# Kernel optimization log

Measured on AMD Instinct MI355X. Metric: run time of the kernel, lower is better.

## Reference

```python
import jax, jax.numpy as jnp
import numpy as np

N = 100000   # nodes
E = 100000   # hyperedges
M = 1600000  # incidences
IN_C = 128
HID = 128
OUT_C = 64
L = 2
EPS = 1e-5


def _layer_norm(x, g, b):
    m = jnp.mean(x, axis=-1, keepdims=True)
    v = jnp.mean((x - m) ** 2, axis=-1, keepdims=True)
    return (x - m) * jax.lax.rsqrt(v + EPS) * g + b


def setup_inputs() -> dict:
    key = jax.random.key(0)
    ks = jax.random.split(key, 16)
    s_in = 1.0 / np.sqrt(IN_C)
    s_h = 1.0 / np.sqrt(HID)
    return {
        "x": jax.random.normal(ks[0], (N, IN_C), jnp.float32),
        "x_e": jax.random.normal(ks[1], (E, IN_C), jnp.float32),
        "edge_index": jax.random.randint(ks[2], (2, M), 0, N, jnp.int32),
        "in_norm_g": jnp.ones((IN_C,), jnp.float32),
        "in_norm_b": jnp.zeros((IN_C,), jnp.float32),
        "in_proj_W": jax.random.normal(ks[3], (IN_C, HID), jnp.float32) * s_in,
        "in_proj_b": jnp.zeros((HID,), jnp.float32),
        "norm_g": jnp.ones((L, HID), jnp.float32),
        "norm_b": jnp.zeros((L, HID), jnp.float32),
        "conv_W": jax.random.normal(ks[4], (L, HID, HID), jnp.float32) * s_h,
        "conv_b": jnp.zeros((L, HID), jnp.float32),
        "lin_W": jax.random.normal(ks[5], (HID, OUT_C), jnp.float32) * s_h,
        "lin_b": jnp.zeros((OUT_C,), jnp.float32),
    }


def reference(x, x_e, edge_index, in_norm_g, in_norm_b, in_proj_W, in_proj_b,
              norm_g, norm_b, conv_W, conv_b, lin_W, lin_b):
    src, dst = edge_index[0], edge_index[1]  # node ids, hyperedge ids
    h = _layer_norm(x, in_norm_g, in_norm_b)
    h = jax.nn.leaky_relu(h @ in_proj_W + in_proj_b)  # dropout = identity (eval)

    # HypergraphConv degree normalizers (hyperedge_weight = 1)
    ones = jnp.ones((M,), h.dtype)
    degD = jax.ops.segment_sum(ones, src, num_segments=N)
    D = jnp.where(degD > 0, 1.0 / degD, 0.0)          # [N]
    degB = jax.ops.segment_sum(ones, dst, num_segments=E)
    B = jnp.where(degB > 0, 1.0 / degB, 0.0)          # [E]

    for i in range(L):
        hn = _layer_norm(h, norm_g[i], norm_b[i])
        xw = hn @ conv_W[i]                            # [N, HID]
        # node -> hyperedge: sum_j B[e] * xw[j]
        he = jax.ops.segment_sum(B[dst][:, None] * xw[src], dst, num_segments=E)
        # hyperedge -> node: sum_e D[n] * he[e]
        h2 = jax.ops.segment_sum(D[src][:, None] * he[dst], src, num_segments=N)
        h = jax.nn.leaky_relu(h2 + conv_b[i])

    # MinAggregation: segment-min of gathered node features per hyperedge
    agg = jax.ops.segment_min(h[src], dst, num_segments=E)  # [E, HID]
    return agg @ lin_W + lin_b                              # [E, OUT_C]
```

## Files before the change

kernel.cpp:

```cpp
#include <hip/hip_runtime.h>

#define NN 100000
#define NE 100000
#define MI 1600000
#define HID 128
#define OUTC 64
#define LSLOPE 0.01f
#define EPSV 1e-5f
#define ADJ_STRIDE 48
#define BUILD_PASSES 10
#define BUILD_WIN ((NN + BUILD_PASSES - 1) / BUILD_PASSES)

typedef __attribute__((ext_vector_type(4))) unsigned short us4;
typedef __attribute__((ext_vector_type(8))) short short8;
typedef __attribute__((ext_vector_type(16))) float f32x16;

__device__ __forceinline__ float bf2f(unsigned short h) {
    return __uint_as_float(((unsigned)h) << 16);
}
__device__ __forceinline__ unsigned short f2bf(float f) {
    unsigned u = __float_as_uint(f);
    return (unsigned short)((u + 0x7FFFu + ((u >> 16) & 1u)) >> 16);
}

__global__ void build_win_kernel(const int* __restrict__ ei,
                                 int* __restrict__ cntE, int* __restrict__ cntN,
                                 int* __restrict__ adjE, int* __restrict__ adjN,
                                 int lo, int hi) {
    int m = blockIdx.x * blockDim.x + threadIdx.x;
    if (m >= MI) return;
    int s = ei[m], d = ei[MI + m];
    if (d >= lo && d < hi) {
        int p = atomicAdd(&cntE[d], 1);
        if (p < ADJ_STRIDE) adjE[d * ADJ_STRIDE + p] = s;
    }
    if (s >= lo && s < hi) {
        int p = atomicAdd(&cntN[s], 1);
        if (p < ADJ_STRIDE) adjN[s * ADJ_STRIDE + p] = d;
    }
}

__global__ void recip_kernel(const int* __restrict__ deg, float* __restrict__ out, int n) {
    int i = blockIdx.x * blockDim.x + threadIdx.x;
    if (i < n) { int d = deg[i]; out[i] = d > 0 ? 1.0f / (float)d : 0.0f; }
}

__global__ void tconv_kernel(const float* __restrict__ src, unsigned short* __restrict__ hi,
                             unsigned short* __restrict__ lo, int K, int N) {
    int idx = blockIdx.x * blockDim.x + threadIdx.x;
    if (idx >= K * N) return;
    int n = idx / K, k = idx - n * K;
    float v = src[k * N + n];
    unsigned short h = f2bf(v);
    hi[idx] = h;
    if (lo) lo[idx] = f2bf(v - bf2f(h));
}

template <int MODE>
__global__ __launch_bounds__(256) void gather_kernel(
    const int* __restrict__ cnt, const int* __restrict__ adj,
    const unsigned short* __restrict__ src, const float* __restrict__ scale,
    const float* __restrict__ bias, unsigned short* __restrict__ dst, int R)
{
    int g = threadIdx.x >> 5;
    int lane = threadIdx.x & 31;
    int r = blockIdx.x * 8 + g;
    if (r >= R) return;
    int n = cnt[r]; n = n < ADJ_STRIDE ? n : ADJ_STRIDE;
    const int* arow = adj + (size_t)r * ADJ_STRIDE;
    float ax, ay, az, aw;
    if (MODE == 2) { ax = ay = az = aw = INFINITY; }
    else           { ax = ay = az = aw = 0.f; }
    const unsigned short* base = src + lane * 4;
    int j = 0;
    for (; j + 3 < n; j += 4) {
        int i0 = arow[j], i1 = arow[j + 1], i2 = arow[j + 2], i3 = arow[j + 3];
        us4 v0 = *(const us4*)(base + (size_t)i0 * HID);
        us4 v1 = *(const us4*)(base + (size_t)i1 * HID);
        us4 v2 = *(const us4*)(base + (size_t)i2 * HID);
        us4 v3 = *(const us4*)(base + (size_t)i3 * HID);
        if (MODE == 2) {
            ax = fminf(ax, fminf(fminf(bf2f(v0.x), bf2f(v1.x)), fminf(bf2f(v2.x), bf2f(v3.x))));
            ay = fminf(ay, fminf(fminf(bf2f(v0.y), bf2f(v1.y)), fminf(bf2f(v2.y), bf2f(v3.y))));
            az = fminf(az, fminf(fminf(bf2f(v0.z), bf2f(v1.z)), fminf(bf2f(v2.z), bf2f(v3.z))));
            aw = fminf(aw, fminf(fminf(bf2f(v0.w), bf2f(v1.w)), fminf(bf2f(v2.w), bf2f(v3.w))));
        } else {
            ax += (bf2f(v0.x) + bf2f(v1.x)) + (bf2f(v2.x) + bf2f(v3.x));
            ay += (bf2f(v0.y) + bf2f(v1.y)) + (bf2f(v2.y) + bf2f(v3.y));
            az += (bf2f(v0.z) + bf2f(v1.z)) + (bf2f(v2.z) + bf2f(v3.z));
            aw += (bf2f(v0.w) + bf2f(v1.w)) + (bf2f(v2.w) + bf2f(v3.w));
        }
    }
    for (; j < n; ++j) {
        int i0 = arow[j];
        us4 v0 = *(const us4*)(base + (size_t)i0 * HID);
        if (MODE == 2) {
            ax = fminf(ax, bf2f(v0.x)); ay = fminf(ay, bf2f(v0.y));
            az = fminf(az, bf2f(v0.z)); aw = fminf(aw, bf2f(v0.w));
        } else {
            ax += bf2f(v0.x); ay += bf2f(v0.y); az += bf2f(v0.z); aw += bf2f(v0.w);
        }
    }
    if (MODE == 0) {
        float s = scale[r];
        ax *= s; ay *= s; az *= s; aw *= s;
    } else if (MODE == 1) {
        float s = scale[r];
        float4 b = *(const float4*)(bias + lane * 4);
        float x;
        x = s * ax + b.x; ax = x > 0.f ? x : LSLOPE * x;
        x = s * ay + b.y; ay = x > 0.f ? x : LSLOPE * x;
        x = s * az + b.z; az = x > 0.f ? x : LSLOPE * x;
        x = s * aw + b.w; aw = x > 0.f ? x : LSLOPE * x;
    }
    us4 o;
    o.x = f2bf(ax); o.y = f2bf(ay); o.z = f2bf(az); o.w = f2bf(aw);
    *(us4*)(dst + (size_t)r * HID + lane * 4) = o;
}

template <int NC, bool ABF16, bool OBF16, bool SPLIT>
__global__ __launch_bounds__(512) void mfma_gemm_kernel(
    const void* __restrict__ Av, const float* __restrict__ ln_g, const float* __restrict__ ln_b,
    const unsigned short* __restrict__ WT, const float* __restrict__ bias,
    void* __restrict__ outv, int R, int flags)
{
    constexpr int SA = 136;
    constexpr int NW = (SPLIT ? 2 : 1) * NC;
    constexpr int CT = NC / 64;
    __shared__ unsigned short As[128 * SA];
    __shared__ unsigned short Ws[NW * SA];
    __shared__ float red_s[512];
    __shared__ float red_q[512];
    __shared__ float r_mean[128];
    __shared__ float r_rstd[128];

    const int t = threadIdx.x;
    const int row0 = blockIdx.x * 128;

    constexpr int WUS4 = NW * 128 / 4;
    #pragma unroll
    for (int i = t; i < WUS4; i += 512) {
        us4 w = ((const us4*)WT)[i];
        int nrow = i >> 5, k4 = i & 31;
        *(us4*)(Ws + nrow * SA + k4 * 4) = w;
    }

    {
        const int r = t >> 2, sub = t & 3;
        const int gr = row0 + r;
        float v[32];
        if (gr < R) {
            if (ABF16) {
                const unsigned short* ap = (const unsigned short*)Av + (size_t)gr * 128 + sub * 32;
                #pragma unroll
                for (int j4 = 0; j4 < 8; ++j4) {
                    us4 x4 = *(const us4*)(ap + j4 * 4);
                    v[j4 * 4 + 0] = bf2f(x4.x); v[j4 * 4 + 1] = bf2f(x4.y);
                    v[j4 * 4 + 2] = bf2f(x4.z); v[j4 * 4 + 3] = bf2f(x4.w);
                }
            } else {
                const float* ap = (const float*)Av + (size_t)gr * 128 + sub * 32;
                #pragma unroll
                for (int j4 = 0; j4 < 8; ++j4) {
                    float4 f4 = *(const float4*)(ap + j4 * 4);
                    v[j4 * 4 + 0] = f4.x; v[j4 * 4 + 1] = f4.y;
                    v[j4 * 4 + 2] = f4.z; v[j4 * 4 + 3] = f4.w;
                }
            }
        } else {
            #pragma unroll
            for (int j = 0; j < 32; ++j) v[j] = 0.f;
        }
        if (flags & 1) {
            float s = 0.f, q = 0.f;
            #pragma unroll
            for (int j = 0; j < 32; ++j) { s += v[j]; q += v[j] * v[j]; }
            red_s[t] = s; red_q[t] = q;
            __syncthreads();
            if (t < 128) {
                float ss = red_s[t * 4] + red_s[t * 4 + 1] + red_s[t * 4 + 2] + red_s[t * 4 + 3];
                float qq = red_q[t * 4] + red_q[t * 4 + 1] + red_q[t * 4 + 2] + red_q[t * 4 + 3];
                float mu = ss * (1.0f / 128.0f);
                float var = qq * (1.0f / 128.0f) - mu * mu;
                r_mean[t] = mu;
                r_rstd[t] = rsqrtf(var + EPSV);
            }
            __syncthreads();
            float mu = r_mean[r], rs = r_rstd[r];
            #pragma unroll
            for (int j4 = 0; j4 < 8; ++j4) {
                float4 g4 = *(const float4*)(ln_g + sub * 32 + j4 * 4);
                float4 b4 = *(const float4*)(ln_b + sub * 32 + j4 * 4);
                v[j4 * 4 + 0] = (v[j4 * 4 + 0] - mu) * rs * g4.x + b4.x;
                v[j4 * 4 + 1] = (v[j4 * 4 + 1] - mu) * rs * g4.y + b4.y;
                v[j4 * 4 + 2] = (v[j4 * 4 + 2] - mu) * rs * g4.z + b4.z;
                v[j4 * 4 + 3] = (v[j4 * 4 + 3] - mu) * rs * g4.w + b4.w;
            }
        }
        #pragma unroll
        for (int j4 = 0; j4 < 8; ++j4) {
            us4 o;
            o.x = f2bf(v[j4 * 4 + 0]); o.y = f2bf(v[j4 * 4 + 1]);
            o.z = f2bf(v[j4 * 4 + 2]); o.w = f2bf(v[j4 * 4 + 3]);
            *(us4*)(As + r * SA + sub * 32 + j4 * 4) = o;
        }
    }
    __syncthreads();

    const int lane = t & 63;
    const int wave = t >> 6;
    const int wr = (wave & 3) * 32;
    const int wc = (wave >> 2) * (NC / 2);
    const int m = lane & 31;
    const int half = lane >> 5;
    const unsigned short* a_base = As + (wr + m) * SA + half * 8;

    f32x16 acc[CT];
    #pragma unroll
    for (int ct = 0; ct < CT; ++ct) acc[ct] = (f32x16)(0.0f);

    #pragma unroll
    for (int ks = 0; ks < 8; ++ks) {
        short8 a = *(const short8*)(a_base + ks * 16);
        #pragma unroll
        for (int ct = 0; ct < CT; ++ct) {
            const unsigned short* b_base = Ws + (wc + ct * 32 + m) * SA + half * 8 + ks * 16;
            short8 b = *(const short8*)b_base;
            acc[ct] = __builtin_amdgcn_mfma_f32_32x32x16_bf16(a, b, acc[ct], 0, 0, 0);
            if (SPLIT) {
                short8 bl = *(const short8*)(b_base + (size_t)NC * SA);
                acc[ct] = __builtin_amdgcn_mfma_f32_32x32x16_bf16(a, bl, acc[ct], 0, 0, 0);
            }
        }
    }

    #pragma unroll
    for (int ct = 0; ct < CT; ++ct) {
        int gc = wc + ct * 32 + m;
        float bv = bias ? bias[gc] : 0.f;
        #pragma unroll
        for (int reg = 0; reg < 16; ++reg) {
            int rloc = (reg & 3) + 8 * (reg >> 2) + 4 * half;
            int gr = row0 + wr + rloc;
            if (gr < R) {
                float y = acc[ct][reg] + bv;
                if (flags & 4) y = y > 0.f ? y : LSLOPE * y;
                if (OBF16) ((unsigned short*)outv)[(size_t)gr * NC + gc] = f2bf(y);
                else       ((float*)outv)[(size_t)gr * NC + gc] = y;
            }
        }
    }
}

extern "C" void kernel_launch(void* const* d_in, const int* in_sizes, int n_in,
                              void* d_out, int out_size, void* d_ws, size_t ws_size,
                              hipStream_t stream) {
    const float* x      = (const float*)d_in[0];
    const int*   ei     = (const int*)d_in[2];
    const float* in_g   = (const float*)d_in[3];
    const float* in_b   = (const float*)d_in[4];
    const float* in_W   = (const float*)d_in[5];
    const float* in_pb  = (const float*)d_in[6];
    const float* norm_g = (const float*)d_in[7];
    const float* norm_b = (const float*)d_in[8];
    const float* conv_W = (const float*)d_in[9];
    const float* conv_b = (const float*)d_in[10];
    const float* lin_W  = (const float*)d_in[11];
    const float* lin_b  = (const float*)d_in[12];
    float* out = (float*)d_out;

    unsigned short* h_bf   = (unsigned short*)d_ws;
    unsigned short* xw_bf  = h_bf  + (size_t)NN * HID;
    unsigned short* he_bf  = xw_bf + (size_t)NN * HID;
    unsigned short* agg_bf = he_bf + (size_t)NE * HID;
    float* D    = (float*)(agg_bf + (size_t)NE * HID);
    float* B    = D + NN;
    int* cntE   = (int*)(B + NE);
    int* cntN   = cntE + NE;
    int* adjE   = cntN + NN;
    int* adjN   = adjE + (size_t)NE * ADJ_STRIDE;
    unsigned short* wt_in  = (unsigned short*)(adjN + (size_t)NN * ADJ_STRIDE);
    unsigned short* wt_c0  = wt_in + 128 * 128;
    unsigned short* wt_c1  = wt_c0 + 128 * 128;
    unsigned short* wt_lin = wt_c1 + 128 * 128;

    hipMemsetAsync(cntE, 0, (size_t)(NN + NE) * sizeof(int), stream);
    for (int p = 0; p < BUILD_PASSES; ++p) {
        int lo = p * BUILD_WIN;
        int hi = lo + BUILD_WIN < NN ? lo + BUILD_WIN : NN;
        build_win_kernel<<<(MI + 255) / 256, 256, 0, stream>>>(ei, cntE, cntN, adjE, adjN, lo, hi);
    }
    recip_kernel<<<(NN + 255) / 256, 256, 0, stream>>>(cntN, D, NN);
    recip_kernel<<<(NE + 255) / 256, 256, 0, stream>>>(cntE, B, NE);

    tconv_kernel<<<(128 * 128 + 255) / 256, 256, 0, stream>>>(in_W, wt_in, nullptr, 128, 128);
    tconv_kernel<<<(128 * 128 + 255) / 256, 256, 0, stream>>>(conv_W, wt_c0, nullptr, 128, 128);
    tconv_kernel<<<(128 * 128 + 255) / 256, 256, 0, stream>>>(conv_W + 128 * 128, wt_c1, nullptr, 128, 128);
    tconv_kernel<<<(128 * 64 + 255) / 256, 256, 0, stream>>>(lin_W, wt_lin, wt_lin + 64 * 128, 128, 64);

    mfma_gemm_kernel<HID, false, true, false><<<(NN + 127) / 128, 512, 0, stream>>>(
        x, in_g, in_b, wt_in, in_pb, h_bf, NN, 1 | 4);

    for (int i = 0; i < 2; ++i) {
        mfma_gemm_kernel<HID, true, true, false><<<(NN + 127) / 128, 512, 0, stream>>>(
            h_bf, norm_g + i * HID, norm_b + i * HID, i ? wt_c1 : wt_c0,
            nullptr, xw_bf, NN, 1);
        gather_kernel<0><<<(NE + 7) / 8, 256, 0, stream>>>(cntE, adjE, xw_bf, B, nullptr, he_bf, NE);
        gather_kernel<1><<<(NN + 7) / 8, 256, 0, stream>>>(cntN, adjN, he_bf, D, conv_b + i * HID, h_bf, NN);
    }

    gather_kernel<2><<<(NE + 7) / 8, 256, 0, stream>>>(cntE, adjE, h_bf, nullptr, nullptr, agg_bf, NE);

    mfma_gemm_kernel<OUTC, true, false, true><<<(NE + 127) / 128, 512, 0, stream>>>(
        agg_bf, nullptr, nullptr, wt_lin, lin_b, out, NE, 0);
}
```

Measured before the change: 809.1 us.

## Store bf16 features in 4 column-chunk planes and gather per chunk

Feature matrices move from row-major [R,128] bf16 to four column-chunk planes of [R,32], so each chunk plane (6.4MB) is more likely to stay in cache during random gathers. The gather kernel now stages adjacency rows and counts in shared memory, processes one 32-column chunk at a time with two half-warps splitting the neighbours, and combines them with a shuffle. The GEMM kernel reads and writes the new layout. Each gather row is now a 64-byte segment, which may fragment memory transactions, and the adjacency list is walked four times.

```diff
diff --git a/kernel.cpp b/kernel.cpp
--- a/kernel.cpp
+++ b/kernel.cpp
@@ -11,17 +11,19 @@
 #define BUILD_PASSES 10
 #define BUILD_WIN ((NN + BUILD_PASSES - 1) / BUILD_PASSES)
 
+typedef unsigned short us;
 typedef __attribute__((ext_vector_type(4))) unsigned short us4;
 typedef __attribute__((ext_vector_type(8))) short short8;
 typedef __attribute__((ext_vector_type(16))) float f32x16;
 
-__device__ __forceinline__ float bf2f(unsigned short h) {
+__device__ __forceinline__ float bf2f(us h) {
     return __uint_as_float(((unsigned)h) << 16);
 }
-__device__ __forceinline__ unsigned short f2bf(float f) {
+__device__ __forceinline__ us f2bf(float f) {
     unsigned u = __float_as_uint(f);
-    return (unsigned short)((u + 0x7FFFu + ((u >> 16) & 1u)) >> 16);
-}
+    return (us)((u + 0x7FFFu + ((u >> 16) & 1u)) >> 16);
+}
+
 
 __global__ void build_win_kernel(const int* __restrict__ ei,
                                  int* __restrict__ cntE, int* __restrict__ cntN,
@@ -45,13 +47,13 @@
     if (i < n) { int d = deg[i]; out[i] = d > 0 ? 1.0f / (float)d : 0.0f; }
 }
 
-__global__ void tconv_kernel(const float* __restrict__ src, unsigned short* __restrict__ hi,
-                             unsigned short* __restrict__ lo, int K, int N) {
+__global__ void tconv_kernel(const float* __restrict__ src, us* __restrict__ hi,
+                             us* __restrict__ lo, int K, int N) {
     int idx = blockIdx.x * blockDim.x + threadIdx.x;
     if (idx >= K * N) return;
     int n = idx / K, k = idx - n * K;
     float v = src[k * N + n];
-    unsigned short h = f2bf(v);
+    us h = f2bf(v);
     hi[idx] = h;
     if (lo) lo[idx] = f2bf(v - bf2f(h));
 }
@@ -59,76 +61,103 @@
 template <int MODE>
 __global__ __launch_bounds__(256) void gather_kernel(
     const int* __restrict__ cnt, const int* __restrict__ adj,
-    const unsigned short* __restrict__ src, const float* __restrict__ scale,
-    const float* __restrict__ bias, unsigned short* __restrict__ dst, int R)
+    const us* __restrict__ src, const float* __restrict__ scale,
+    const float* __restrict__ bias, us* __restrict__ dst, int R)
 {
-    int g = threadIdx.x >> 5;
-    int lane = threadIdx.x & 31;
-    int r = blockIdx.x * 8 + g;
+    __shared__ int s_adj[8][ADJ_STRIDE];
+    __shared__ int s_cnt[8];
+    __shared__ float s_scale[8];
+
+    const int t = threadIdx.x;
+    const int r0 = blockIdx.x * 8;
+
+    if (t < 8) {
+        int r = r0 + t;
+        int n = 0; float sc = 0.f;
+        if (r < R) {
+            n = cnt[r]; n = n < ADJ_STRIDE ? n : ADJ_STRIDE;
+            if (MODE != 2 && scale) sc = scale[r];
+        }
+        s_cnt[t] = n;
+        s_scale[t] = sc;
+    }
+    for (int i = t; i < 8 * ADJ_STRIDE; i += 256) {
+        int lr = i / ADJ_STRIDE, k = i - lr * ADJ_STRIDE;
+        if (r0 + lr < R) s_adj[lr][k] = adj[(size_t)(r0 + lr) * ADJ_STRIDE + k];
+    }
+    __syncthreads();
+
+    const int g = t >> 5;
+    const int lane = t & 31;
+    const int r = r0 + g;
     if (r >= R) return;
-    int n = cnt[r]; n = n < ADJ_STRIDE ? n : ADJ_STRIDE;
-    const int* arow = adj + (size_t)r * ADJ_STRIDE;
-    float ax, ay, az, aw;
-    if (MODE == 2) { ax = ay = az = aw = INFINITY; }
-    else           { ax = ay = az = aw = 0.f; }
-    const unsigned short* base = src + lane * 4;
-    int j = 0;
-    for (; j + 3 < n; j += 4) {
-        int i0 = arow[j], i1 = arow[j + 1], i2 = arow[j + 2], i3 = arow[j + 3];
-        us4 v0 = *(const us4*)(base + (size_t)i0 * HID);
-        us4 v1 = *(const us4*)(base + (size_t)i1 * HID);
-        us4 v2 = *(const us4*)(base + (size_t)i2 * HID);
-        us4 v3 = *(const us4*)(base + (size_t)i3 * HID);
-        if (MODE == 2) {
-            ax = fminf(ax, fminf(fminf(bf2f(v0.x), bf2f(v1.x)), fminf(bf2f(v2.x), bf2f(v3.x))));
-            ay = fminf(ay, fminf(fminf(bf2f(v0.y), bf2f(v1.y)), fminf(bf2f(v2.y), bf2f(v3.y))));
-            az = fminf(az, fminf(fminf(bf2f(v0.z), bf2f(v1.z)), fminf(bf2f(v2.z), bf2f(v3.z))));
-            aw = fminf(aw, fminf(fminf(bf2f(v0.w), bf2f(v1.w)), fminf(bf2f(v2.w), bf2f(v3.w))));
-        } else {
-            ax += (bf2f(v0.x) + bf2f(v1.x)) + (bf2f(v2.x) + bf2f(v3.x));
-            ay += (bf2f(v0.y) + bf2f(v1.y)) + (bf2f(v2.y) + bf2f(v3.y));
-            az += (bf2f(v0.z) + bf2f(v1.z)) + (bf2f(v2.z) + bf2f(v3.z));
-            aw += (bf2f(v0.w) + bf2f(v1.w)) + (bf2f(v2.w) + bf2f(v3.w));
-        }
-    }
-    for (; j < n; ++j) {
-        int i0 = arow[j];
-        us4 v0 = *(const us4*)(base + (size_t)i0 * HID);
-        if (MODE == 2) {
-            ax = fminf(ax, bf2f(v0.x)); ay = fminf(ay, bf2f(v0.y));
-            az = fminf(az, bf2f(v0.z)); aw = fminf(aw, bf2f(v0.w));
-        } else {
-            ax += bf2f(v0.x); ay += bf2f(v0.y); az += bf2f(v0.z); aw += bf2f(v0.w);
-        }
-    }
-    if (MODE == 0) {
-        float s = scale[r];
-        ax *= s; ay *= s; az *= s; aw *= s;
-    } else if (MODE == 1) {
-        float s = scale[r];
-        float4 b = *(const float4*)(bias + lane * 4);
-        float x;
-        x = s * ax + b.x; ax = x > 0.f ? x : LSLOPE * x;
-        x = s * ay + b.y; ay = x > 0.f ? x : LSLOPE * x;
-        x = s * az + b.z; az = x > 0.f ? x : LSLOPE * x;
-        x = s * aw + b.w; aw = x > 0.f ? x : LSLOPE * x;
-    }
-    us4 o;
-    o.x = f2bf(ax); o.y = f2bf(ay); o.z = f2bf(az); o.w = f2bf(aw);
-    *(us4*)(dst + (size_t)r * HID + lane * 4) = o;
-}
-
-template <int NC, bool ABF16, bool OBF16, bool SPLIT>
+    const int n = s_cnt[g];
+    const int eh = lane >> 4;
+    const int cl = lane & 15;
+    const int* arow = s_adj[g];
+
+    #pragma unroll
+    for (int c = 0; c < 4; ++c) {
+        const us* sbase = src + (size_t)c * R * 32 + cl * 2;
+        float a0, a1;
+        if (MODE == 2) { a0 = a1 = INFINITY; } else { a0 = a1 = 0.f; }
+        int j = eh;
+        for (; j + 6 < n; j += 8) {
+            unsigned v0 = *(const unsigned*)(sbase + (size_t)arow[j]     * 32);
+            unsigned v1 = *(const unsigned*)(sbase + (size_t)arow[j + 2] * 32);
+            unsigned v2 = *(const unsigned*)(sbase + (size_t)arow[j + 4] * 32);
+            unsigned v3 = *(const unsigned*)(sbase + (size_t)arow[j + 6] * 32);
+            float f0a = bf2f((us)v0), f0b = bf2f((us)(v0 >> 16));
+            float f1a = bf2f((us)v1), f1b = bf2f((us)(v1 >> 16));
+            float f2a = bf2f((us)v2), f2b = bf2f((us)(v2 >> 16));
+            float f3a = bf2f((us)v3), f3b = bf2f((us)(v3 >> 16));
+            if (MODE == 2) {
+                a0 = fminf(a0, fminf(fminf(f0a, f1a), fminf(f2a, f3a)));
+                a1 = fminf(a1, fminf(fminf(f0b, f1b), fminf(f2b, f3b)));
+            } else {
+                a0 += (f0a + f1a) + (f2a + f3a);
+                a1 += (f0b + f1b) + (f2b + f3b);
+            }
+        }
+        for (; j < n; j += 2) {
+            unsigned v0 = *(const unsigned*)(sbase + (size_t)arow[j] * 32);
+            float f0a = bf2f((us)v0), f0b = bf2f((us)(v0 >> 16));
+            if (MODE == 2) { a0 = fminf(a0, f0a); a1 = fminf(a1, f0b); }
+            else           { a0 += f0a; a1 += f0b; }
+        }
+        float b0 = __shfl_xor(a0, 16);
+        float b1 = __shfl_xor(a1, 16);
+        if (MODE == 2) { a0 = fminf(a0, b0); a1 = fminf(a1, b1); }
+        else           { a0 += b0; a1 += b1; }
+
+        if (eh == 0) {
+            if (MODE == 0) {
+                float s = s_scale[g];
+                a0 *= s; a1 *= s;
+            } else if (MODE == 1) {
+                float s = s_scale[g];
+                float2 bb = *(const float2*)(bias + c * 32 + cl * 2);
+                float x;
+                x = s * a0 + bb.x; a0 = x > 0.f ? x : LSLOPE * x;
+                x = s * a1 + bb.y; a1 = x > 0.f ? x : LSLOPE * x;
+            }
+            unsigned o = (unsigned)f2bf(a0) | ((unsigned)f2bf(a1) << 16);
+            *(unsigned*)(dst + ((size_t)c * R + r) * 32 + cl * 2) = o;
+        }
+    }
+}
+
+template <int NC, int ALAY, bool OBF16, bool SPLIT>
 __global__ __launch_bounds__(512) void mfma_gemm_kernel(
     const void* __restrict__ Av, const float* __restrict__ ln_g, const float* __restrict__ ln_b,
-    const unsigned short* __restrict__ WT, const float* __restrict__ bias,
+    const us* __restrict__ WT, const float* __restrict__ bias,
     void* __restrict__ outv, int R, int flags)
 {
     constexpr int SA = 136;
     constexpr int NW = (SPLIT ? 2 : 1) * NC;
     constexpr int CT = NC / 64;
-    __shared__ unsigned short As[128 * SA];
-    __shared__ unsigned short Ws[NW * SA];
+    __shared__ us As[128 * SA];
+    __shared__ us Ws[NW * SA];
     __shared__ float red_s[512];
     __shared__ float red_q[512];
     __shared__ float r_mean[128];
@@ -150,8 +179,8 @@
         const int gr = row0 + r;
         float v[32];
         if (gr < R) {
-            if (ABF16) {
-                const unsigned short* ap = (const unsigned short*)Av + (size_t)gr * 128 + sub * 32;
+            if (ALAY == 1) {
+                const us* ap = (const us*)Av + ((size_t)sub * R + gr) * 32;
                 #pragma unroll
                 for (int j4 = 0; j4 < 8; ++j4) {
                     us4 x4 = *(const us4*)(ap + j4 * 4);
@@ -213,7 +242,7 @@
     const int wc = (wave >> 2) * (NC / 2);
     const int m = lane & 31;
     const int half = lane >> 5;
-    const unsigned short* a_base = As + (wr + m) * SA + half * 8;
+    const us* a_base = As + (wr + m) * SA + half * 8;
 
     f32x16 acc[CT];
     #pragma unroll
@@ -224,7 +253,7 @@
         short8 a = *(const short8*)(a_base + ks * 16);
         #pragma unroll
         for (int ct = 0; ct < CT; ++ct) {
-            const unsigned short* b_base = Ws + (wc + ct * 32 + m) * SA + half * 8 + ks * 16;
+            const us* b_base = Ws + (wc + ct * 32 + m) * SA + half * 8 + ks * 16;
             short8 b = *(const short8*)b_base;
             acc[ct] = __builtin_amdgcn_mfma_f32_32x32x16_bf16(a, b, acc[ct], 0, 0, 0);
             if (SPLIT) {
@@ -245,8 +274,10 @@
             if (gr < R) {
                 float y = acc[ct][reg] + bv;
                 if (flags & 4) y = y > 0.f ? y : LSLOPE * y;
-                if (OBF16) ((unsigned short*)outv)[(size_t)gr * NC + gc] = f2bf(y);
-                else       ((float*)outv)[(size_t)gr * NC + gc] = y;
+                if (OBF16)
+                    ((us*)outv)[((size_t)(gc >> 5) * R + gr) * 32 + (gc & 31)] = f2bf(y);
+                else
+                    ((float*)outv)[(size_t)gr * NC + gc] = y;
             }
         }
     }
@@ -269,20 +300,20 @@
     const float* lin_b  = (const float*)d_in[12];
     float* out = (float*)d_out;
 
-    unsigned short* h_bf   = (unsigned short*)d_ws;
-    unsigned short* xw_bf  = h_bf  + (size_t)NN * HID;
-    unsigned short* he_bf  = xw_bf + (size_t)NN * HID;
-    unsigned short* agg_bf = he_bf + (size_t)NE * HID;
+    us* h_bf   = (us*)d_ws;
+    us* xw_bf  = h_bf  + (size_t)NN * HID;
+    us* he_bf  = xw_bf + (size_t)NN * HID;
+    us* agg_bf = he_bf + (size_t)NE * HID;
     float* D    = (float*)(agg_bf + (size_t)NE * HID);
     float* B    = D + NN;
     int* cntE   = (int*)(B + NE);
     int* cntN   = cntE + NE;
     int* adjE   = cntN + NN;
     int* adjN   = adjE + (size_t)NE * ADJ_STRIDE;
-    unsigned short* wt_in  = (unsigned short*)(adjN + (size_t)NN * ADJ_STRIDE);
-    unsigned short* wt_c0  = wt_in + 128 * 128;
-    unsigned short* wt_c1  = wt_c0 + 128 * 128;
-    unsigned short* wt_lin = wt_c1 + 128 * 128;
+    us* wt_in  = (us*)(adjN + (size_t)NN * ADJ_STRIDE);
+    us* wt_c0  = wt_in + 128 * 128;
+    us* wt_c1  = wt_c0 + 128 * 128;
+    us* wt_lin = wt_c1 + 128 * 128;
 
     hipMemsetAsync(cntE, 0, (size_t)(NN + NE) * sizeof(int), stream);
     for (int p = 0; p < BUILD_PASSES; ++p) {
@@ -298,11 +329,11 @@
     tconv_kernel<<<(128 * 128 + 255) / 256, 256, 0, stream>>>(conv_W + 128 * 128, wt_c1, nullptr, 128, 128);
     tconv_kernel<<<(128 * 64 + 255) / 256, 256, 0, stream>>>(lin_W, wt_lin, wt_lin + 64 * 128, 128, 64);
 
-    mfma_gemm_kernel<HID, false, true, false><<<(NN + 127) / 128, 512, 0, stream>>>(
+    mfma_gemm_kernel<HID, 0, true, false><<<(NN + 127) / 128, 512, 0, stream>>>(
         x, in_g, in_b, wt_in, in_pb, h_bf, NN, 1 | 4);
 
     for (int i = 0; i < 2; ++i) {
-        mfma_gemm_kernel<HID, true, true, false><<<(NN + 127) / 128, 512, 0, stream>>>(
+        mfma_gemm_kernel<HID, 1, true, false><<<(NN + 127) / 128, 512, 0, stream>>>(
             h_bf, norm_g + i * HID, norm_b + i * HID, i ? wt_c1 : wt_c0,
             nullptr, xw_bf, NN, 1);
         gather_kernel<0><<<(NE + 7) / 8, 256, 0, stream>>>(cntE, adjE, xw_bf, B, nullptr, he_bf, NE);
@@ -311,6 +342,6 @@
 
     gather_kernel<2><<<(NE + 7) / 8, 256, 0, stream>>>(cntE, adjE, h_bf, nullptr, nullptr, agg_bf, NE);
 
-    mfma_gemm_kernel<OUTC, true, false, true><<<(NE + 127) / 128, 512, 0, stream>>>(
+    mfma_gemm_kernel<OUTC, 1, false, true><<<(NE + 127) / 128, 512, 0, stream>>>(
         agg_bf, nullptr, nullptr, wt_lin, lin_b, out, NE, 0);
 }
```

Result: slower. 1.011 ms (+25.0%).
